# Kernel tuning notes

Measured on AMD Instinct MI355X. Metric: run time of the kernel, lower is better.

## Reference

```python
import jax, jax.numpy as jnp
import numpy as np

N = 100000
E = 3200000
D = 64


def setup_inputs() -> dict:
    key = jax.random.key(0)
    k1, k2, k3 = jax.random.split(key, 3)
    indices = jax.random.randint(k1, (2, E), 0, N, dtype=jnp.int64) if jax.config.jax_enable_x64 else jax.random.randint(k1, (2, E), 0, N, dtype=jnp.int32)
    values = jax.random.uniform(k2, (E,), dtype=jnp.float32)
    b = jax.random.normal(k3, (N, D), dtype=jnp.float32)
    return {"indices": indices, "values": values, "shape": N, "b": b}


def reference(indices, values, shape, b):
    # sparse COO [N,N] @ dense [N,D]:
    # out[r] = sum over edges e with row[e]==r of values[e] * b[col[e]]
    row, col = indices[0], indices[1]
    msgs = values[:, None] * b[col]            # [E, D] gather + scale
    out = jax.ops.segment_sum(msgs, row, num_segments=shape)  # [N, D] scatter-add
    return out
```

## Files before the change

### kernel.cpp

```cpp
#include <hip/hip_runtime.h>
#include <hip/hip_bf16.h>


#define D 64
#define BROWS 64
#define MAXNB 2048
#define CAP 2560
#define LPSZ (CAP + 192)
#define NM (CAP / 256)
#define SPILLCAP 8192
#define NCHUNK 4
#define NBINS (BROWS * NCHUNK)

#define CROWS 2048
#define NCB 64
#define SCH_A 4096
#define CBLK 4352
#define NBLK_C 16
#define CAPC (CBLK * NBLK_C)

__global__ __launch_bounds__(256) void spmm_atomic_kernel(
    const int* __restrict__ rows, const int* __restrict__ cols,
    const float* __restrict__ vals, const float* __restrict__ b,
    float* __restrict__ out, int E) {
  long long gid = (long long)blockIdx.x * blockDim.x + threadIdx.x;
  int e = (int)(gid >> 6);
  int d = (int)(gid & 63);
  if (e >= E) return;
  atomicAdd(&out[(long long)rows[e] * D + d], vals[e] * b[(long long)cols[e] * D + d]);
}

__device__ __forceinline__ unsigned bf16rne(float x) {
  unsigned u = __float_as_uint(x);
  return (u + 0x7FFFu + ((u >> 16) & 1u)) >> 16;
}
__global__ __launch_bounds__(256) void convert_kernel(
    const float4* __restrict__ src, uint2* __restrict__ dst, int n4) {
  int i = blockIdx.x * 256 + threadIdx.x;
  if (i >= n4) return;
  float4 f = src[i];
  dst[i] = make_uint2(bf16rne(f.x) | (bf16rne(f.y) << 16),
                      bf16rne(f.z) | (bf16rne(f.w) << 16));
}

__global__ __launch_bounds__(256) void coarse_scatter_kernel(
    const int* __restrict__ rows, const int* __restrict__ cols,
    const float* __restrict__ vals, int* __restrict__ gcoarse,
    uint2* __restrict__ cslab_lo, uint2* __restrict__ cslab_hi, int csplit,
    uint4* __restrict__ spill, int* __restrict__ spill_cnt, int E) {
  __shared__ uint2 stage[SCH_A];
  __shared__ unsigned char sbin[SCH_A];
  __shared__ int h[NCB];
  __shared__ int lst[NCB];
  __shared__ int gb[NCB];
  int t = threadIdx.x;
  if (t < NCB) h[t] = 0;
  __syncthreads();
  int start = blockIdx.x * SCH_A;
  int ec = E - start;
  if (ec > SCH_A) ec = SCH_A;
  bool full = (start + SCH_A <= E);

  int4 r4[4];
  int rank[16];
  if (full) {
#pragma unroll
    for (int ki = 0; ki < 4; ki++) {
      r4[ki] = ((const int4*)(rows + start + ki * 1024))[t];
      rank[4 * ki + 0] = atomicAdd(&h[r4[ki].x >> 11], 1);
      rank[4 * ki + 1] = atomicAdd(&h[r4[ki].y >> 11], 1);
      rank[4 * ki + 2] = atomicAdd(&h[r4[ki].z >> 11], 1);
      rank[4 * ki + 3] = atomicAdd(&h[r4[ki].w >> 11], 1);
    }
  } else {
#pragma unroll
    for (int ki = 0; ki < 4; ki++) {
      int e = start + ki * 1024 + t * 4;
      int4 rr = make_int4(-1, -1, -1, -1);
      if (e + 0 < E) { rr.x = rows[e + 0]; rank[4 * ki + 0] = atomicAdd(&h[rr.x >> 11], 1); }
      if (e + 1 < E) { rr.y = rows[e + 1]; rank[4 * ki + 1] = atomicAdd(&h[rr.y >> 11], 1); }
      if (e + 2 < E) { rr.z = rows[e + 2]; rank[4 * ki + 2] = atomicAdd(&h[rr.z >> 11], 1); }
      if (e + 3 < E) { rr.w = rows[e + 3]; rank[4 * ki + 3] = atomicAdd(&h[rr.w >> 11], 1); }
      r4[ki] = rr;
    }
  }
  __syncthreads();
  if (t < NCB) {
    int c = h[t];
    int x = c;
#pragma unroll
    for (int off = 1; off < 64; off <<= 1) {
      int u = __shfl_up(x, off);
      if (t >= off) x += u;
    }
    lst[t] = x - c;
    gb[t] = c ? atomicAdd(&gcoarse[t], c) : 0;
  }
  __syncthreads();
#pragma unroll
  for (int ki = 0; ki < 4; ki++) {
    int e = start + ki * 1024 + t * 4;
    int rr[4] = {r4[ki].x, r4[ki].y, r4[ki].z, r4[ki].w};
    int cc[4];
    float vv[4];
    if (full) {
      int4 c4 = ((const int4*)(cols + start + ki * 1024))[t];
      float4 v4 = ((const float4*)(vals + start + ki * 1024))[t];
      cc[0] = c4.x; cc[1] = c4.y; cc[2] = c4.z; cc[3] = c4.w;
      vv[0] = v4.x; vv[1] = v4.y; vv[2] = v4.z; vv[3] = v4.w;
    } else {
#pragma unroll
      for (int j = 0; j < 4; j++) {
        cc[j] = (e + j < E) ? cols[e + j] : 0;
        vv[j] = (e + j < E) ? vals[e + j] : 0.f;
      }
    }
#pragma unroll
    for (int j = 0; j < 4; j++) {
      if (e + j < E) {
        int r = rr[j];
        int bn = r >> 11;
        int pos = lst[bn] + rank[4 * ki + j];
        stage[pos] = make_uint2(((unsigned)(r & (CROWS - 1)) << 17) |
                                    (unsigned)cc[j],
                                __float_as_uint(vv[j]));
        sbin[pos] = (unsigned char)bn;
      }
    }
  }
  __syncthreads();
  for (int i = t; i < ec; i += 256) {
    int bn = sbin[i];
    uint2 p = stage[i];
    int pin = gb[bn] + (i - lst[bn]);
    if (pin < CAPC) {
      uint2* slab = (bn < csplit) ? (cslab_lo + (size_t)bn * CAPC)
                                  : (cslab_hi + (size_t)(bn - csplit) * CAPC);
      slab[pin] = p;
    } else {
      int sp = atomicAdd(spill_cnt, 1);
      if (sp < SPILLCAP)
        spill[sp] = make_uint4((unsigned)((bn << 11) | (int)(p.x >> 17)),
                               p.x & 0x1FFFFu, p.y, 0u);
    }
  }
}

__global__ __launch_bounds__(256) void fine_scatter_kernel(
    const int* __restrict__ gcoarse, const uint2* __restrict__ cslab_lo,
    const uint2* __restrict__ cslab_hi, int csplit, int* __restrict__ gcount,
    uint2* __restrict__ pairs, uint4* __restrict__ spill,
    int* __restrict__ spill_cnt) {
  int c = blockIdx.x >> 4;
  int blk = blockIdx.x & 15;
  int cnt = gcoarse[c];
  if (cnt > CAPC) cnt = CAPC;
  int base = blk * CBLK;
  int ec = cnt - base;
  if (ec <= 0) return;
  if (ec > CBLK) ec = CBLK;
  const uint2* src = ((c < csplit) ? (cslab_lo + (size_t)c * CAPC)
                                   : (cslab_hi + (size_t)(c - csplit) * CAPC)) +
                     base;
  __shared__ uint2 stage[CBLK];
  __shared__ unsigned char sbin[CBLK];
  __shared__ int h[32];
  __shared__ int lst[32];
  __shared__ int gb[32];
  int t = threadIdx.x;
  if (t < 32) h[t] = 0;
  __syncthreads();
  uint2 mine[17];
  int rank[17];
#pragma unroll
  for (int k = 0; k < 17; k++) {
    int i = k * 256 + t;
    if (i < ec) {
      mine[k] = src[i];
      rank[k] = atomicAdd(&h[mine[k].x >> 23], 1);
    }
  }
  __syncthreads();
  if (t < 32) {
    int cn = h[t];
    int x = cn;
#pragma unroll
    for (int off = 1; off < 32; off <<= 1) {
      int u = __shfl_up(x, off);
      if (t >= off) x += u;
    }
    lst[t] = x - cn;
    gb[t] = cn ? atomicAdd(&gcount[c * 32 + t], cn) : 0;
  }
  __syncthreads();
#pragma unroll
  for (int k = 0; k < 17; k++) {
    int i = k * 256 + t;
    if (i < ec) {
      uint2 p = mine[k];
      int f = (int)(p.x >> 23);
      int pos = lst[f] + rank[k];
      unsigned key2 = (((p.x >> 17) & 63u) << 26) | ((p.x & 0x1FFFFu) << 7);
      stage[pos] = make_uint2(key2, p.y);
      sbin[pos] = (unsigned char)f;
    }
  }
  __syncthreads();
  for (int i = t; i < ec; i += 256) {
    int f = sbin[i];
    uint2 p = stage[i];
    int pin = gb[f] + (i - lst[f]);
    int gbkt = c * 32 + f;
    if (pin < CAP) {
      pairs[(size_t)gbkt * CAP + pin] = p;
    } else {
      int sp = atomicAdd(spill_cnt, 1);
      if (sp < SPILLCAP)
        spill[sp] = make_uint4((unsigned)(gbkt * BROWS + (int)(p.x >> 26)),
                               (p.x >> 7) & 0x1FFFFu, p.y, 0u);
    }
  }
}

__global__ __launch_bounds__(256) void spmm_fused_kernel(
    const uint2* __restrict__ pairs, const int* __restrict__ gcount,
    const uint2* __restrict__ b16, float* __restrict__ out, int N) {
  __shared__ uint2 lp[LPSZ];
  __shared__ int cnt[NBINS];
  __shared__ int roff[NBINS + 1];
  __shared__ int rreal[BROWS];
  int bkt = blockIdx.x;
  int cntE = gcount[bkt];
  if (cntE > CAP) cntE = CAP;
  const uint2* src = pairs + (size_t)bkt * CAP;
  int t = threadIdx.x;
  if (t < NBINS) cnt[t] = 0;
  __syncthreads();
  uint2 mine[NM];
  int rk[NM];
#pragma unroll
  for (int k = 0; k < NM; k++) {
    int i = t + k * 256;
    if (i < cntE) {
      mine[k] = src[i];
      int bin = ((mine[k].x >> 26) << 2) | ((mine[k].x >> 22) & 3);
      rk[k] = atomicAdd(&cnt[bin], 1);
    }
  }
  __syncthreads();
  if (t < BROWS) {
    int c0 = cnt[4 * t + 0], c1 = cnt[4 * t + 1];
    int c2 = cnt[4 * t + 2], c3 = cnt[4 * t + 3];
    int s = c0 + c1 + c2 + c3;
    int pad = (s + 3) & ~3;
    int x = pad;
#pragma unroll
    for (int off = 1; off < 64; off <<= 1) {
      int u = __shfl_up(x, off);
      if (t >= off) x += u;
    }
    int base = x - pad;
    roff[4 * t + 0] = base;
    roff[4 * t + 1] = base + c0;
    roff[4 * t + 2] = base + c0 + c1;
    roff[4 * t + 3] = base + c0 + c1 + c2;
    rreal[t] = base + s;
    if (t == BROWS - 1) roff[NBINS] = x;
  }
  __syncthreads();
#pragma unroll
  for (int k = 0; k < NM; k++) {
    int i = t + k * 256;
    if (i < cntE) {
      int bin = ((mine[k].x >> 26) << 2) | ((mine[k].x >> 22) & 3);
      lp[roff[bin] + rk[k]] = make_uint2(mine[k].x & 0x03FFFF80u, mine[k].y);
    }
  }
  if (t < BROWS) {
    int e0 = rreal[t], e1 = roff[4 * t + 4];
    for (int i = e0; i < e1; i++) lp[i] = make_uint2(0u, 0u);
  }
  __syncthreads();
  int lane = t & 63;
  int wv = t >> 6;
  int g = lane >> 3;
  int l8 = lane & 7;
  int gid32 = wv * 8 + g;
  const char* bq = (const char*)b16 + (l8 << 4);
  int row_base = bkt * BROWS;
  float2 acc[2][4];
#pragma unroll
  for (int rr = 0; rr < 2; rr++)
#pragma unroll
    for (int j = 0; j < 4; j++) acc[rr][j] = make_float2(0.f, 0.f);
#pragma unroll
  for (int rr = 0; rr < 2; rr++) {
    int r = gid32 + 32 * rr;
    int j0 = roff[r << 2], j1 = roff[(r << 2) + 4];
    for (int base = j0; base < j1; base += 4) {
      uint4 bv[4];
      float vv[4];
#pragma unroll
      for (int k = 0; k < 4; k++) {
        uint2 p = lp[base + k];
        bv[k] = *(const uint4*)(bq + p.x);
        vv[k] = __uint_as_float(p.y);
      }
#pragma unroll
      for (int k = 0; k < 4; k++) {
        unsigned u0 = bv[k].x, u1 = bv[k].y, u2 = bv[k].z, u3 = bv[k].w;
        float v = vv[k];
        acc[rr][0].x += v * __uint_as_float(u0 << 16);
        acc[rr][0].y += v * __uint_as_float(u0 & 0xFFFF0000u);
        acc[rr][1].x += v * __uint_as_float(u1 << 16);
        acc[rr][1].y += v * __uint_as_float(u1 & 0xFFFF0000u);
        acc[rr][2].x += v * __uint_as_float(u2 << 16);
        acc[rr][2].y += v * __uint_as_float(u2 & 0xFFFF0000u);
        acc[rr][3].x += v * __uint_as_float(u3 << 16);
        acc[rr][3].y += v * __uint_as_float(u3 & 0xFFFF0000u);
      }
    }
  }
#pragma unroll
  for (int rr = 0; rr < 2; rr++) {
    int gr = row_base + gid32 + 32 * rr;
    if (gr < N) {
      float4* dst = (float4*)(out + (size_t)gr * D + l8 * 8);
      dst[0] = make_float4(acc[rr][0].x, acc[rr][0].y, acc[rr][1].x, acc[rr][1].y);
      dst[1] = make_float4(acc[rr][2].x, acc[rr][2].y, acc[rr][3].x, acc[rr][3].y);
    }
  }
}

__global__ __launch_bounds__(256) void spill_fix_kernel(
    const uint4* __restrict__ spill, const int* __restrict__ spill_cnt,
    const float* __restrict__ b, float* __restrict__ out) {
  int n = *spill_cnt;
  if (n > SPILLCAP) n = SPILLCAP;
  int lane = threadIdx.x & 63;
  int w = (int)((blockIdx.x * blockDim.x + threadIdx.x) >> 6);
  int nw = (int)((gridDim.x * blockDim.x) >> 6);
  for (int s = w; s < n; s += nw) {
    uint4 e = spill[s];
    atomicAdd(&out[(size_t)e.x * D + lane],
              __uint_as_float(e.z) * b[(size_t)e.y * D + lane]);
  }
}

extern "C" void kernel_launch(void* const* d_in, const int* in_sizes, int n_in,
                              void* d_out, int out_size, void* d_ws, size_t ws_size,
                              hipStream_t stream) {
  const int* indices = (const int*)d_in[0];
  const float* vals  = (const float*)d_in[1];
  const float* b     = (const float*)d_in[3];

  int E = in_sizes[1];
  int N = in_sizes[3] / D;
  const int* rows = indices;
  const int* cols = indices + E;

  int NC = (N + CROWS - 1) / CROWS;
  int n4 = N * D / 4;

  size_t off_gcount  = 0;
  size_t off_gcoarse = off_gcount + (size_t)MAXNB * 4;
  size_t off_scnt    = off_gcoarse + (size_t)NCB * 4;
  size_t off_spill   = (off_scnt + 4 + 15) & ~(size_t)15;
  size_t off_pairs   = off_spill + (size_t)SPILLCAP * 16;
  size_t npbkt       = (size_t)NC * 32;
  size_t off_b16     = off_pairs + npbkt * CAP * 8;
  size_t off_cextra  = off_b16 + (size_t)N * D * 2;
  size_t outbytes    = (size_t)out_size * 4;
  int csplit = (int)(outbytes / ((size_t)CAPC * 8));
  if (csplit > NC) csplit = NC;
  size_t cextra = (size_t)(NC - csplit) * CAPC * 8;
  size_t need2 = off_cextra + cextra;

  if (ws_size >= need2 && NC <= NCB && (int)npbkt <= MAXNB) {
    char*  ws        = (char*)d_ws;
    int*   gcount    = (int*)(ws + off_gcount);
    int*   gcoarse   = (int*)(ws + off_gcoarse);
    int*   spill_cnt = (int*)(ws + off_scnt);
    uint4* spill     = (uint4*)(ws + off_spill);
    uint2* pairs     = (uint2*)(ws + off_pairs);
    uint2* b16       = (uint2*)(ws + off_b16);
    uint2* cslab_lo  = (uint2*)d_out;
    uint2* cslab_hi  = (uint2*)(ws + off_cextra);

    hipMemsetAsync(gcount, 0, (size_t)MAXNB * 4 + (size_t)NCB * 4 + 4, stream);
    convert_kernel<<<(n4 + 255) / 256, 256, 0, stream>>>(
        (const float4*)b, b16, n4);
    coarse_scatter_kernel<<<(E + SCH_A - 1) / SCH_A, 256, 0, stream>>>(
        rows, cols, vals, gcoarse, cslab_lo, cslab_hi, csplit,
        spill, spill_cnt, E);
    fine_scatter_kernel<<<NC * NBLK_C, 256, 0, stream>>>(
        gcoarse, cslab_lo, cslab_hi, csplit, gcount, pairs, spill, spill_cnt);
    spmm_fused_kernel<<<(int)npbkt, 256, 0, stream>>>(pairs, gcount, b16,
                                                      (float*)d_out, N);
    spill_fix_kernel<<<16, 256, 0, stream>>>(spill, spill_cnt, b,
                                             (float*)d_out);
    return;
  }

  hipMemsetAsync(d_out, 0, (size_t)out_size * sizeof(float), stream);
  long long total = (long long)E * 64;
  spmm_atomic_kernel<<<(int)((total + 255) / 256), 256, 0, stream>>>(
      rows, cols, vals, b, (float*)d_out, E);
}
```

Baseline: 230.5 us.

## Fuse bf16 conversion into coarse scatter and fold spill fix into SpMM

The standalone b-to-bf16 conversion kernel is merged into the coarse scatter launch as extra trailing blocks, so the two run concurrently in one launch. The separate spill_fix atomic kernel is removed; each SpMM block now scans the spill list and adds its own rows' spilled edges, using bf16 b. The per-row zero padding of LDS segments is replaced by a full 256-bin prefix scan with per-chunk loops that mask tail elements. This cuts two launches and the padding pass, but every block now reads the spill counter and may loop over the whole spill list, and the tail masking adds work per segment.

```diff
diff --git a/kernel.cpp b/kernel.cpp
--- a/kernel.cpp
+++ b/kernel.cpp
@@ -6,7 +6,6 @@
 #define BROWS 64
 #define MAXNB 2048
 #define CAP 2560
-#define LPSZ (CAP + 192)
 #define NM (CAP / 256)
 #define SPILLCAP 8192
 #define NCHUNK 4
@@ -18,6 +17,7 @@
 #define CBLK 4352
 #define NBLK_C 16
 #define CAPC (CBLK * NBLK_C)
+#define NCONV 1024
 
 __global__ __launch_bounds__(256) void spmm_atomic_kernel(
     const int* __restrict__ rows, const int* __restrict__ cols,
@@ -34,26 +34,28 @@
   unsigned u = __float_as_uint(x);
   return (u + 0x7FFFu + ((u >> 16) & 1u)) >> 16;
 }
-__global__ __launch_bounds__(256) void convert_kernel(
-    const float4* __restrict__ src, uint2* __restrict__ dst, int n4) {
-  int i = blockIdx.x * 256 + threadIdx.x;
-  if (i >= n4) return;
-  float4 f = src[i];
-  dst[i] = make_uint2(bf16rne(f.x) | (bf16rne(f.y) << 16),
-                      bf16rne(f.z) | (bf16rne(f.w) << 16));
-}
-
-__global__ __launch_bounds__(256) void coarse_scatter_kernel(
+__global__ __launch_bounds__(256) void coarse_conv_kernel(
     const int* __restrict__ rows, const int* __restrict__ cols,
     const float* __restrict__ vals, int* __restrict__ gcoarse,
     uint2* __restrict__ cslab_lo, uint2* __restrict__ cslab_hi, int csplit,
-    uint4* __restrict__ spill, int* __restrict__ spill_cnt, int E) {
+    uint4* __restrict__ spill, int* __restrict__ spill_cnt, int E, int nco,
+    const float4* __restrict__ bsrc, uint2* __restrict__ b16, int n4) {
   __shared__ uint2 stage[SCH_A];
   __shared__ unsigned char sbin[SCH_A];
   __shared__ int h[NCB];
   __shared__ int lst[NCB];
   __shared__ int gb[NCB];
   int t = threadIdx.x;
+
+  if (blockIdx.x >= nco) {
+    for (int i = (blockIdx.x - nco) * 256 + t; i < n4; i += NCONV * 256) {
+      float4 f = bsrc[i];
+      b16[i] = make_uint2(bf16rne(f.x) | (bf16rne(f.y) << 16),
+                          bf16rne(f.z) | (bf16rne(f.w) << 16));
+    }
+    return;
+  }
+
   if (t < NCB) h[t] = 0;
   __syncthreads();
   int start = blockIdx.x * SCH_A;
@@ -224,16 +226,19 @@
 
 __global__ __launch_bounds__(256) void spmm_fused_kernel(
     const uint2* __restrict__ pairs, const int* __restrict__ gcount,
-    const uint2* __restrict__ b16, float* __restrict__ out, int N) {
-  __shared__ uint2 lp[LPSZ];
+    const uint2* __restrict__ b16, float* __restrict__ out, int N,
+    const uint4* __restrict__ spill, const int* __restrict__ spill_cnt) {
+  __shared__ uint2 lp[CAP];
   __shared__ int cnt[NBINS];
   __shared__ int roff[NBINS + 1];
-  __shared__ int rreal[BROWS];
+  __shared__ int wpart[4];
   int bkt = blockIdx.x;
   int cntE = gcount[bkt];
   if (cntE > CAP) cntE = CAP;
   const uint2* src = pairs + (size_t)bkt * CAP;
   int t = threadIdx.x;
+  int lane = t & 63;
+  int wv = t >> 6;
   if (t < NBINS) cnt[t] = 0;
   __syncthreads();
   uint2 mine[NM];
@@ -248,24 +253,20 @@
     }
   }
   __syncthreads();
-  if (t < BROWS) {
-    int c0 = cnt[4 * t + 0], c1 = cnt[4 * t + 1];
-    int c2 = cnt[4 * t + 2], c3 = cnt[4 * t + 3];
-    int s = c0 + c1 + c2 + c3;
-    int pad = (s + 3) & ~3;
-    int x = pad;
+  {
+    int c0 = cnt[t];
+    int x = c0;
 #pragma unroll
     for (int off = 1; off < 64; off <<= 1) {
       int u = __shfl_up(x, off);
-      if (t >= off) x += u;
-    }
-    int base = x - pad;
-    roff[4 * t + 0] = base;
-    roff[4 * t + 1] = base + c0;
-    roff[4 * t + 2] = base + c0 + c1;
-    roff[4 * t + 3] = base + c0 + c1 + c2;
-    rreal[t] = base + s;
-    if (t == BROWS - 1) roff[NBINS] = x;
+      if (lane >= off) x += u;
+    }
+    if (lane == 63) wpart[wv] = x;
+    __syncthreads();
+    int wbase = 0;
+    for (int w = 0; w < wv; w++) wbase += wpart[w];
+    roff[t] = wbase + x - c0;
+    if (t == 255) roff[NBINS] = wbase + x;
   }
   __syncthreads();
 #pragma unroll
@@ -276,48 +277,70 @@
       lp[roff[bin] + rk[k]] = make_uint2(mine[k].x & 0x03FFFF80u, mine[k].y);
     }
   }
-  if (t < BROWS) {
-    int e0 = rreal[t], e1 = roff[4 * t + 4];
-    for (int i = e0; i < e1; i++) lp[i] = make_uint2(0u, 0u);
-  }
-  __syncthreads();
-  int lane = t & 63;
-  int wv = t >> 6;
+  __syncthreads();
   int g = lane >> 3;
   int l8 = lane & 7;
   int gid32 = wv * 8 + g;
   const char* bq = (const char*)b16 + (l8 << 4);
   int row_base = bkt * BROWS;
-  float2 acc[2][4];
-#pragma unroll
-  for (int rr = 0; rr < 2; rr++)
-#pragma unroll
-    for (int j = 0; j < 4; j++) acc[rr][j] = make_float2(0.f, 0.f);
-#pragma unroll
-  for (int rr = 0; rr < 2; rr++) {
-    int r = gid32 + 32 * rr;
-    int j0 = roff[r << 2], j1 = roff[(r << 2) + 4];
-    for (int base = j0; base < j1; base += 4) {
-      uint4 bv[4];
-      float vv[4];
-#pragma unroll
-      for (int k = 0; k < 4; k++) {
-        uint2 p = lp[base + k];
-        bv[k] = *(const uint4*)(bq + p.x);
-        vv[k] = __uint_as_float(p.y);
+  float acc[2][8] = {{0.f, 0.f, 0.f, 0.f, 0.f, 0.f, 0.f, 0.f},
+                     {0.f, 0.f, 0.f, 0.f, 0.f, 0.f, 0.f, 0.f}};
+  for (int ch = 0; ch < NCHUNK; ch++) {
+#pragma unroll
+    for (int rr = 0; rr < 2; rr++) {
+      int r = gid32 + 32 * rr;
+      int bin = (r << 2) | ch;
+      int j0 = roff[bin], j1 = roff[bin + 1];
+      for (int base = j0; base < j1; base += 4) {
+        uint4 bv[4];
+        float vv[4];
+#pragma unroll
+        for (int k = 0; k < 4; k++) {
+          int idx = base + k;
+          int ic = (idx < j1) ? idx : j0;
+          uint2 p = lp[ic];
+          bv[k] = *(const uint4*)(bq + p.x);
+          vv[k] = (idx < j1) ? __uint_as_float(p.y) : 0.f;
+        }
+#pragma unroll
+        for (int k = 0; k < 4; k++) {
+          unsigned u0 = bv[k].x, u1 = bv[k].y, u2 = bv[k].z, u3 = bv[k].w;
+          float v = vv[k];
+          acc[rr][0] += v * __uint_as_float(u0 << 16);
+          acc[rr][1] += v * __uint_as_float(u0 & 0xFFFF0000u);
+          acc[rr][2] += v * __uint_as_float(u1 << 16);
+          acc[rr][3] += v * __uint_as_float(u1 & 0xFFFF0000u);
+          acc[rr][4] += v * __uint_as_float(u2 << 16);
+          acc[rr][5] += v * __uint_as_float(u2 & 0xFFFF0000u);
+          acc[rr][6] += v * __uint_as_float(u3 << 16);
+          acc[rr][7] += v * __uint_as_float(u3 & 0xFFFF0000u);
+        }
       }
-#pragma unroll
-      for (int k = 0; k < 4; k++) {
-        unsigned u0 = bv[k].x, u1 = bv[k].y, u2 = bv[k].z, u3 = bv[k].w;
-        float v = vv[k];
-        acc[rr][0].x += v * __uint_as_float(u0 << 16);
-        acc[rr][0].y += v * __uint_as_float(u0 & 0xFFFF0000u);
-        acc[rr][1].x += v * __uint_as_float(u1 << 16);
-        acc[rr][1].y += v * __uint_as_float(u1 & 0xFFFF0000u);
-        acc[rr][2].x += v * __uint_as_float(u2 << 16);
-        acc[rr][2].y += v * __uint_as_float(u2 & 0xFFFF0000u);
-        acc[rr][3].x += v * __uint_as_float(u3 << 16);
-        acc[rr][3].y += v * __uint_as_float(u3 & 0xFFFF0000u);
+    }
+  }
+  int nsp = *spill_cnt;
+  if (nsp > 0) {
+    if (nsp > SPILLCAP) nsp = SPILLCAP;
+    for (int s = 0; s < nsp; s++) {
+      uint4 e = spill[s];
+      int rg = (int)e.x;
+      if ((rg >> 6) != bkt) continue;
+      int rl = rg & 63;
+#pragma unroll
+      for (int rr = 0; rr < 2; rr++) {
+        if (rl == gid32 + 32 * rr) {
+          uint4 bv = *(const uint4*)((const char*)b16 +
+                                     ((size_t)e.y << 7) + (l8 << 4));
+          float v = __uint_as_float(e.z);
+          acc[rr][0] += v * __uint_as_float(bv.x << 16);
+          acc[rr][1] += v * __uint_as_float(bv.x & 0xFFFF0000u);
+          acc[rr][2] += v * __uint_as_float(bv.y << 16);
+          acc[rr][3] += v * __uint_as_float(bv.y & 0xFFFF0000u);
+          acc[rr][4] += v * __uint_as_float(bv.z << 16);
+          acc[rr][5] += v * __uint_as_float(bv.z & 0xFFFF0000u);
+          acc[rr][6] += v * __uint_as_float(bv.w << 16);
+          acc[rr][7] += v * __uint_as_float(bv.w & 0xFFFF0000u);
+        }
       }
     }
   }
@@ -326,24 +349,9 @@
     int gr = row_base + gid32 + 32 * rr;
     if (gr < N) {
       float4* dst = (float4*)(out + (size_t)gr * D + l8 * 8);
-      dst[0] = make_float4(acc[rr][0].x, acc[rr][0].y, acc[rr][1].x, acc[rr][1].y);
-      dst[1] = make_float4(acc[rr][2].x, acc[rr][2].y, acc[rr][3].x, acc[rr][3].y);
-    }
-  }
-}
-
-__global__ __launch_bounds__(256) void spill_fix_kernel(
-    const uint4* __restrict__ spill, const int* __restrict__ spill_cnt,
-    const float* __restrict__ b, float* __restrict__ out) {
-  int n = *spill_cnt;
-  if (n > SPILLCAP) n = SPILLCAP;
-  int lane = threadIdx.x & 63;
-  int w = (int)((blockIdx.x * blockDim.x + threadIdx.x) >> 6);
-  int nw = (int)((gridDim.x * blockDim.x) >> 6);
-  for (int s = w; s < n; s += nw) {
-    uint4 e = spill[s];
-    atomicAdd(&out[(size_t)e.x * D + lane],
-              __uint_as_float(e.z) * b[(size_t)e.y * D + lane]);
+      dst[0] = make_float4(acc[rr][0], acc[rr][1], acc[rr][2], acc[rr][3]);
+      dst[1] = make_float4(acc[rr][4], acc[rr][5], acc[rr][6], acc[rr][7]);
+    }
   }
 }
 
@@ -388,17 +396,14 @@
     uint2* cslab_hi  = (uint2*)(ws + off_cextra);
 
     hipMemsetAsync(gcount, 0, (size_t)MAXNB * 4 + (size_t)NCB * 4 + 4, stream);
-    convert_kernel<<<(n4 + 255) / 256, 256, 0, stream>>>(
-        (const float4*)b, b16, n4);
-    coarse_scatter_kernel<<<(E + SCH_A - 1) / SCH_A, 256, 0, stream>>>(
+    int nco = (E + SCH_A - 1) / SCH_A;
+    coarse_conv_kernel<<<nco + NCONV, 256, 0, stream>>>(
         rows, cols, vals, gcoarse, cslab_lo, cslab_hi, csplit,
-        spill, spill_cnt, E);
+        spill, spill_cnt, E, nco, (const float4*)b, b16, n4);
     fine_scatter_kernel<<<NC * NBLK_C, 256, 0, stream>>>(
         gcoarse, cslab_lo, cslab_hi, csplit, gcount, pairs, spill, spill_cnt);
-    spmm_fused_kernel<<<(int)npbkt, 256, 0, stream>>>(pairs, gcount, b16,
-                                                      (float*)d_out, N);
-    spill_fix_kernel<<<16, 256, 0, stream>>>(spill, spill_cnt, b,
-                                             (float*)d_out);
+    spmm_fused_kernel<<<(int)npbkt, 256, 0, stream>>>(
+        pairs, gcount, b16, (float*)d_out, N, spill, spill_cnt);
     return;
   }
 
```

Measured after the change: 215.8 us. 6.4% less time.
